# Kernel tuning notes

Measured on AMD Instinct MI355X. Metric: run time of the kernel, lower is better.

The kernel has to match this reference:

```python
import jax, jax.numpy as jnp
import numpy as np

B, S, N, F, H = 8, 12, 4096, 4, 64  # batch, seq_len, num_nodes, input_dim, hidden_dim


def setup_inputs() -> dict:
    key = jax.random.key(0)
    ks = jax.random.split(key, 16)
    sc = 0.05
    adj = jax.random.uniform(ks[0], (N, N), jnp.float32) * (2.0 / N)  # ~row-normalized Laplacian
    return {
        "X": jax.random.normal(ks[1], (B, S, N, F), jnp.float32),
        "adj": adj,
        "struc_emb": jax.random.normal(ks[2], (N, H), jnp.float32),
        "W1": jax.random.normal(ks[3], (H + F, 3 * H), jnp.float32) * sc,
        "b1": jnp.ones((3 * H,), jnp.float32),  # bias=1.0 init in graph_conv1
        "W2": jax.random.normal(ks[4], (H + F, H), jnp.float32) * sc,
        "b2": jnp.zeros((H,), jnp.float32),
        "W_ih": jax.random.normal(ks[5], (4 * H, H), jnp.float32) * sc,
        "W_hh": jax.random.normal(ks[6], (4 * H, H), jnp.float32) * sc,
        "b_ih": jnp.zeros((4 * H,), jnp.float32),
        "b_hh": jnp.zeros((4 * H,), jnp.float32),
        "D1": jax.random.normal(ks[7], (H, H // 2), jnp.float32) * sc,
        "bd1": jnp.zeros((H // 2,), jnp.float32),
        "D2": jax.random.normal(ks[8], (H // 2, 1), jnp.float32) * sc,
        "bd2": jnp.zeros((1,), jnp.float32),
    }


def _graph_conv(adj, x_t, h_flat, W, b, out_dim):
    # x_t: [B,N,F]; h_flat: [B, N*H]
    h = h_flat.reshape(B, N, H)
    cat = jnp.concatenate([x_t, h], axis=-1)            # [B,N,F+H]
    a = jnp.einsum('mn,bnf->bmf', adj, cat)             # laplacian diffusion
    out = a @ W + b                                     # [B,N,out_dim]
    return out.reshape(B, N * out_dim)


def reference(X, adj, struc_emb, W1, b1, W2, b2, W_ih, W_hh, b_ih, b_hh, D1, bd1, D2, bd2):
    # ---- encoder: TGTCCellLSTM unrolled over time (cell_state never updated, as in source) ----
    h0 = jnp.broadcast_to(struc_emb.reshape(1, N * H), (B, N * H))
    c0 = h0  # cell returns old cell_state, so it stays the struc_emb forever (faithful)

    def enc_step(h, x_t):
        g = jax.nn.sigmoid(_graph_conv(adj, x_t, h, W1, b1, 3 * H))   # [B, N*3H]
        f, i, o = jnp.split(g, 3, axis=1)                             # flat chunk, as in torch code
        conv = _graph_conv(adj, x_t, h, W2, b2, H)                    # [B, N*H]
        c = f * c0 + i * jnp.tanh(conv)
        h_new = o * jnp.tanh(c)
        return h_new, None

    h_last, _ = jax.lax.scan(enc_step, h0, jnp.swapaxes(X, 0, 1))  # scan over S
    z = h_last.reshape(B, N, H)

    # ---- decoder: 1-layer LSTM fed the same z at every step, then 2-layer MLP to scalar ----
    x_dec = z.reshape(B * N, H)
    x_gates = x_dec @ W_ih.T + b_ih + b_hh  # input contribution constant across steps

    def dec_step(carry, _):
        h, c = carry
        gates = x_gates + h @ W_hh.T
        i, f, g, o = jnp.split(gates, 4, axis=1)  # torch LSTM gate order
        c = jax.nn.sigmoid(f) * c + jax.nn.sigmoid(i) * jnp.tanh(g)
        h = jax.nn.sigmoid(o) * jnp.tanh(c)
        return (h, c), h

    zeros = jnp.zeros((B * N, H), X.dtype)
    _, hs = jax.lax.scan(dec_step, (zeros, zeros), None, length=S)  # [S, B*N, H]
    hs = jnp.swapaxes(hs, 0, 1)                                      # [B*N, S, H]
    d = jax.nn.relu(hs @ D1 + bd1) @ D2 + bd2                        # [B*N, S, 1]
    recon = d.reshape(B, S, N)  # flat reshape from (B*N, S), matching torch reshape semantics
    return (z, recon)
```

## Files before the change

### kernel.cpp

```cpp
#include <hip/hip_runtime.h>
#include <cstdint>
#include <cstddef>


typedef unsigned short u16;
typedef short s8v __attribute__((ext_vector_type(8)));
typedef unsigned short h8v __attribute__((ext_vector_type(8)));
typedef float f4v __attribute__((ext_vector_type(4)));
typedef int   i4v __attribute__((ext_vector_type(4)));

__device__ __forceinline__ u16 f2bf(float x){
  union { float f; uint32_t u; } v; v.f = x;
  uint32_t r = v.u + 0x7FFFu + ((v.u >> 16) & 1u);
  return (u16)(r >> 16);
}
__device__ __forceinline__ float bf2f(u16 x){
  union { uint32_t u; float f; } v; v.u = ((uint32_t)x) << 16; return v.f;
}
__device__ __forceinline__ float frcp(float x){ return __builtin_amdgcn_rcpf(x); }
__device__ __forceinline__ float fsig(float x){ return frcp(1.0f + __expf(-x)); }
__device__ __forceinline__ float ftanh(float x){ return 1.0f - 2.0f * frcp(1.0f + __expf(2.0f * x)); }
__device__ __forceinline__ int8_t f2i8(float x){
  int v = (int)rintf(x);
  v = v > 127 ? 127 : (v < -127 ? -127 : v);
  return (int8_t)v;
}

typedef const __attribute__((address_space(1))) unsigned int* gp_t;
typedef __attribute__((address_space(3))) unsigned int* lp_t;
__device__ __forceinline__ void glds16(const void* g, void* l){
  __builtin_amdgcn_global_load_lds((gp_t)g, (lp_t)l, 16, 0, 0);
}

__global__ __launch_bounds__(256)
void gemm_s1_i8(const int8_t* __restrict__ A, const int8_t* __restrict__ Bt,
                u16* __restrict__ Cpart, int Ncols, int ksl, float cscale)
{
  __shared__ int8_t As[2 * 128 * 128];
  __shared__ int8_t Bs[2 * 128 * 128];
  const int t  = threadIdx.x;
  const int l  = t & 63;
  const int w  = t >> 6;
  const int wm = (w >> 1) * 64;
  const int wc = (w & 1) * 64;
  const int mb = blockIdx.x * 128;
  const int nb = blockIdx.y * 128;
  const int k0 = blockIdx.z * ksl;

  i4v acc[4][4];
  #pragma unroll
  for (int i = 0; i < 4; ++i)
    #pragma unroll
    for (int j = 0; j < 4; ++j) acc[i][j] = (i4v)0;

  const int srow = t >> 3;
  const int gsw  = ((t & 7) ^ (srow & 7)) * 16;
  const int8_t* ab = A  + (size_t)(mb + srow) * 4096 + k0 + gsw;
  const int8_t* bb = Bt + (size_t)(nb + srow) * 4096 + k0 + gsw;

  const int rA = l & 15;
  const int lsw = l & 7;

  #pragma unroll
  for (int j = 0; j < 4; ++j) {
    glds16(ab + (size_t)(32 * j) * 4096, As + j * 4096 + t * 16);
    glds16(bb + (size_t)(32 * j) * 4096, Bs + j * 4096 + t * 16);
  }

  for (int kk = 0; kk < ksl; kk += 128) {
    const int cur = (kk >> 7) & 1;
    __syncthreads();
    if (kk + 128 < ksl) {
      const int nxt = cur ^ 1;
      #pragma unroll
      for (int j = 0; j < 4; ++j) {
        glds16(ab + (size_t)(32 * j) * 4096 + kk + 128, As + nxt * 16384 + j * 4096 + t * 16);
        glds16(bb + (size_t)(32 * j) * 4096 + kk + 128, Bs + nxt * 16384 + j * 4096 + t * 16);
      }
    }
    const int bofs = cur * 16384;
    #pragma unroll
    for (int sub = 0; sub < 2; ++sub) {
      const int kpos = ((sub * 4 + (l >> 4)) ^ lsw) * 16;
      i4v af[4], bf[4];
      #pragma unroll
      for (int mt = 0; mt < 4; ++mt)
        af[mt] = *(const i4v*)&As[bofs + (wm + mt * 16 + rA) * 128 + kpos];
      #pragma unroll
      for (int nt = 0; nt < 4; ++nt)
        bf[nt] = *(const i4v*)&Bs[bofs + (wc + nt * 16 + rA) * 128 + kpos];
      #pragma unroll
      for (int mt = 0; mt < 4; ++mt)
        #pragma unroll
        for (int nt = 0; nt < 4; ++nt)
          acc[mt][nt] = __builtin_amdgcn_mfma_i32_16x16x64_i8(af[mt], bf[nt], acc[mt][nt], 0, 0, 0);
    }
  }

  u16* Cs = Cpart + (size_t)blockIdx.z * 4096 * Ncols;
  const int colo = l & 15;
  const int rowo = (l >> 4) * 4;
  #pragma unroll
  for (int mt = 0; mt < 4; ++mt)
    #pragma unroll
    for (int nt = 0; nt < 4; ++nt)
      #pragma unroll
      for (int r = 0; r < 4; ++r) {
        int gr = mb + wm + mt * 16 + rowo + r;
        int gc = nb + wc + nt * 16 + colo;
        Cs[(size_t)gr * Ncols + gc] = f2bf((float)acc[mt][nt][r] * cscale);
      }
}

__global__ __launch_bounds__(256)
void reduceN(const u16* __restrict__ P, u16* __restrict__ O, size_t SL)
{
  size_t i = ((size_t)blockIdx.x * 256 + threadIdx.x) * 8;
  if (i >= SL) return;
  float s[8] = {0,0,0,0,0,0,0,0};
  #pragma unroll
  for (int z = 0; z < 4; ++z) {
    uint4 v = *(const uint4*)(P + z * SL + i);
    uint32_t wd[4] = {v.x, v.y, v.z, v.w};
    #pragma unroll
    for (int q = 0; q < 4; ++q) {
      union { uint32_t u; float f; } lo, hi;
      lo.u = wd[q] << 16; hi.u = wd[q] & 0xFFFF0000u;
      s[2*q] += lo.f; s[2*q+1] += hi.f;
    }
  }
  uint4 o; uint32_t* ow = (uint32_t*)&o;
  #pragma unroll
  for (int q = 0; q < 4; ++q)
    ow[q] = (uint32_t)f2bf(s[2*q]) | ((uint32_t)f2bf(s[2*q+1]) << 16);
  *(uint4*)(O + i) = o;
}

__global__ __launch_bounds__(256)
void gemm_s2(const u16* __restrict__ AH, const u16* __restrict__ AXb,
             const u16* __restrict__ WT, const float* __restrict__ b1v,
             const float* __restrict__ b2v, u16* __restrict__ G, int tstep)
{
  __shared__ u16 As[64*104];
  __shared__ u16 Bs[256*104];
  const int t = threadIdx.x;
  const int l = t & 63, w = t >> 6;
  const int wm = (w >> 1) * 32, wc0 = (w & 1) * 32;
  const int mb = blockIdx.x * 64;
  const size_t SL = 32768ull * 64;

  #pragma unroll
  for (int pass = 0; pass < 2; ++pass) {
    int idx = t + pass * 256;
    int row = idx >> 3, oct = idx & 7;
    size_t base = (size_t)(mb + row) * 64 + oct * 8;
    float s[8] = {0,0,0,0,0,0,0,0};
    #pragma unroll
    for (int z = 0; z < 4; ++z) {
      uint4 v = *(const uint4*)(AH + z * SL + base);
      uint32_t wd[4] = {v.x, v.y, v.z, v.w};
      #pragma unroll
      for (int q = 0; q < 4; ++q) {
        union { uint32_t u; float f; } lo, hi;
        lo.u = wd[q] << 16; hi.u = wd[q] & 0xFFFF0000u;
        s[2*q] += lo.f; s[2*q+1] += hi.f;
      }
    }
    uint4 o; uint32_t* ow = (uint32_t*)&o;
    #pragma unroll
    for (int q = 0; q < 4; ++q)
      ow[q] = (uint32_t)f2bf(s[2*q]) | ((uint32_t)f2bf(s[2*q+1]) << 16);
    *(uint4*)&As[row * 104 + oct * 8] = o;
  }
  {
    int row = t >> 2, q = t & 3;
    uint4 o = {0, 0, 0, 0};
    if (q == 0) {
      int r = mb + row, n = r >> 3, b = r & 7;
      const uint32_t* src = (const uint32_t*)(AXb + (size_t)n * 384 + tstep * 32 + b * 4);
      o.x = src[0]; o.y = src[1];
    }
    *(uint4*)&As[row * 104 + 64 + q * 8] = o;
  }
  #pragma unroll
  for (int pass = 0; pass < 12; ++pass) {
    int idx = t + pass * 256;
    int row = idx / 12, seg = idx - row * 12;
    *(uint4*)&Bs[row * 104 + seg * 8] = *(const uint4*)(WT + (size_t)row * 96 + seg * 8);
  }
  __syncthreads();

  const int rA = l & 15, kg = (l >> 4) * 8;
  s8v af[3][2];
  #pragma unroll
  for (int kc = 0; kc < 3; ++kc)
    #pragma unroll
    for (int mt = 0; mt < 2; ++mt)
      af[kc][mt] = *(const s8v*)&As[(wm + mt * 16 + rA) * 104 + kc * 32 + kg];

  const int colo = l & 15, rowo = (l >> 4) * 4;
  #pragma unroll
  for (int nb4 = 0; nb4 < 4; ++nb4) {
    const int wc = nb4 * 64 + wc0;
    f4v acc[2][2];
    #pragma unroll
    for (int i = 0; i < 2; ++i)
      #pragma unroll
      for (int j = 0; j < 2; ++j) acc[i][j] = (f4v)0.0f;
    #pragma unroll
    for (int kc = 0; kc < 3; ++kc) {
      s8v bf[2];
      #pragma unroll
      for (int nt = 0; nt < 2; ++nt)
        bf[nt] = *(const s8v*)&Bs[(wc + nt * 16 + rA) * 104 + kc * 32 + kg];
      #pragma unroll
      for (int mt = 0; mt < 2; ++mt)
        #pragma unroll
        for (int nt = 0; nt < 2; ++nt)
          acc[mt][nt] = __builtin_amdgcn_mfma_f32_16x16x32_bf16(af[kc][mt], bf[nt], acc[mt][nt], 0, 0, 0);
    }

    #pragma unroll
    for (int mt = 0; mt < 2; ++mt)
      #pragma unroll
      for (int nt = 0; nt < 2; ++nt) {
        int gc = wc + nt * 16 + colo;
        float bb = (gc < 192) ? b1v[gc] : b2v[gc - 192];
        #pragma unroll
        for (int r = 0; r < 4; ++r) {
          int gr = mb + wm + mt * 16 + rowo + r;
          int np = gr >> 3, b = gr & 7;
          float v = acc[mt][nt][r] + bb;
          size_t addr;
          u16 val;
          if (gc < 192) {
            int p = np * 192 + gc;
            int role = p >> 18;
            int k = p & 262143;
            addr = ((size_t)(role * 8 + b) << 18) + k;
            val = f2bf(fsig(v));
          } else {
            int k = np * 64 + (gc - 192);
            addr = ((size_t)(24 + b) << 18) + k;
            val = f2bf(ftanh(v));
          }
          G[addr] = val;
        }
      }
  }
}

__global__ void conv_adj_i8(const float* __restrict__ adj, int8_t* __restrict__ out){
  size_t i = ((size_t)blockIdx.x * 256 + threadIdx.x) * 4;
  float4 v = *(const float4*)(adj + i);
  const float s = 127.0f * 2048.0f;
  char4 o;
  o.x = f2i8(v.x * s); o.y = f2i8(v.y * s); o.z = f2i8(v.z * s); o.w = f2i8(v.w * s);
  *(char4*)(out + i) = o;
}

__global__ void build_w(const float* __restrict__ W1, const float* __restrict__ W2,
                        const float* __restrict__ Wih, const float* __restrict__ Whh,
                        const float* __restrict__ D1,
                        u16* __restrict__ WT, u16* __restrict__ WihB,
                        u16* __restrict__ WhhB, u16* __restrict__ D1t){
  int gid = blockIdx.x * 256 + threadIdx.x;
  if (gid < 24576) {
    int j = gid / 96, ch = gid - j * 96;
    float v = 0.0f;
    int rr = (ch < 64) ? (ch + 4) : (ch < 68 ? ch - 64 : -1);
    if (rr >= 0) v = (j < 192) ? W1[(size_t)rr * 192 + j] : W2[(size_t)rr * 64 + (j - 192)];
    WT[gid] = f2bf(v);
  } else if (gid < 40960) {
    int q = gid - 24576; WihB[q] = f2bf(Wih[q]);
  } else if (gid < 57344) {
    int q = gid - 40960; WhhB[q] = f2bf(Whh[q]);
  } else if (gid < 59392) {
    int q = gid - 57344;
    int j = q >> 6, hh = q & 63;
    D1t[q] = f2bf(D1[(size_t)hh * 32 + j]);
  }
}

__global__ void init_pb(const float* __restrict__ struc, int8_t* __restrict__ PB){
  int gid = blockIdx.x * 256 + threadIdx.x;
  int n = gid & 4095;
  int r = gid >> 12;
  int hh = r & 63;
  PB[(size_t)r * 4096 + n] = f2i8(struc[(size_t)n * 64 + hh] * 25.4f);
}

__global__ void pack_xall(const float* __restrict__ X, int8_t* __restrict__ Xp){
  int gid = blockIdx.x * 256 + threadIdx.x;
  int n = gid & 4095;
  int col = gid >> 12;
  int ts = col >> 5, r = col & 31, b = r >> 2, f = r & 3;
  Xp[(size_t)col * 4096 + n] = f2i8(X[(((size_t)(b * 12 + ts)) * 4096 + n) * 4 + f] * 25.4f);
}

__global__ __launch_bounds__(256)
void enc_update(const u16* __restrict__ G, const float* __restrict__ struc,
                int8_t* __restrict__ PB, float* __restrict__ zout,
                u16* __restrict__ zbf, int last)
{
  __shared__ uint8_t hx[64 * 40];
  const int t = threadIdx.x;
  const int b = blockIdx.x >> 7;
  const int n0 = (blockIdx.x & 127) * 32;
  const int k8 = n0 * 64 + t * 8;
  const int nloc = t >> 3;
  const int hh0 = (t & 7) * 8;

  h8v f8 = *(const h8v*)&G[((size_t)(     b) << 18) + k8];
  h8v i8_ = *(const h8v*)&G[((size_t)( 8 + b) << 18) + k8];
  h8v o8 = *(const h8v*)&G[((size_t)(16 + b) << 18) + k8];
  h8v c8 = *(const h8v*)&G[((size_t)(24 + b) << 18) + k8];
  float4 s0 = *(const float4*)&struc[k8];
  float4 s1 = *(const float4*)&struc[k8 + 4];
  float sv[8] = {s0.x, s0.y, s0.z, s0.w, s1.x, s1.y, s1.z, s1.w};

  float hv[8];
  #pragma unroll
  for (int j = 0; j < 8; ++j) {
    float c = bf2f(f8[j]) * sv[j] + bf2f(i8_[j]) * bf2f(c8[j]);
    hv[j] = bf2f(o8[j]) * ftanh(c);
    hx[(hh0 + j) * 40 + nloc] = (uint8_t)f2i8(hv[j] * 127.0f);
  }
  if (last) {
    float4 z0 = {hv[0], hv[1], hv[2], hv[3]};
    float4 z1 = {hv[4], hv[5], hv[6], hv[7]};
    *(float4*)&zout[((size_t)b << 18) + k8] = z0;
    *(float4*)&zout[((size_t)b << 18) + k8 + 4] = z1;
    h8v zb;
    #pragma unroll
    for (int j = 0; j < 8; ++j) zb[j] = f2bf(hv[j]);
    *(h8v*)&zbf[((size_t)b << 18) + k8] = zb;
  }
  __syncthreads();
  {
    int row = t >> 2, seg = t & 3;
    uint2 v = *(const uint2*)&hx[row * 40 + seg * 8];
    *(uint2*)&PB[(size_t)(b * 64 + row) * 4096 + n0 + seg * 8] = v;
  }
}

__global__ __launch_bounds__(512, 4)
void dec_fused(const u16* __restrict__ zbf, const u16* __restrict__ WihB,
               const u16* __restrict__ WhhB,
               const float* __restrict__ bih, const float* __restrict__ bhh,
               const u16* __restrict__ D1t, const float* __restrict__ bd1,
               const float* __restrict__ D2, const float* __restrict__ bd2,
               float* __restrict__ recon)
{
  __shared__ u16 whl[256 * 72];
  __shared__ u16 hl[64 * 72];
  const int t = threadIdx.x;
  const int l = t & 63;
  const int w = t >> 6;
  const int wg = w >> 1;
  const int half = w & 1;
  const int r0 = blockIdx.x * 64;
  const int rA = l & 15;
  const int kg = (l >> 4) * 8;

  for (int c = t; c < 2048; c += 512) {
    int j = c >> 3, k8 = (c & 7) * 8;
    *(uint4*)&whl[j * 72 + k8] = *(const uint4*)&WhhB[j * 64 + k8];
  }

  f4v xg[8];
  {
    s8v a0 = *(const s8v*)&zbf[(size_t)(r0 + wg * 16 + rA) * 64 + kg];
    s8v a1 = *(const s8v*)&zbf[(size_t)(r0 + wg * 16 + rA) * 64 + 32 + kg];
    #pragma unroll
    for (int j = 0; j < 8; ++j) {
      int nt = (j >> 1) * 4 + half * 2 + (j & 1);
      s8v b0 = *(const s8v*)&WihB[(nt * 16 + rA) * 64 + kg];
      s8v b1 = *(const s8v*)&WihB[(nt * 16 + rA) * 64 + 32 + kg];
      f4v a = (f4v)0.0f;
      a = __builtin_amdgcn_mfma_f32_16x16x32_bf16(a0, b0, a, 0, 0, 0);
      a = __builtin_amdgcn_mfma_f32_16x16x32_bf16(a1, b1, a, 0, 0, 0);
      float bb = bih[nt * 16 + rA] + bhh[nt * 16 + rA];
      #pragma unroll
      for (int r = 0; r < 4; ++r) xg[j][r] = a[r] + bb;
    }
  }
  s8v d1f[4];
  #pragma unroll
  for (int nt2 = 0; nt2 < 2; ++nt2)
    #pragma unroll
    for (int kc = 0; kc < 2; ++kc)
      d1f[nt2 * 2 + kc] = *(const s8v*)&D1t[(nt2 * 16 + rA) * 64 + kc * 32 + kg];
  const float bd1x = bd1[rA], bd1y = bd1[16 + rA];
  const float d2x = D2[rA], d2y = D2[16 + rA];
  const float bd2v = bd2[0];

  float cst[8];
  #pragma unroll
  for (int q = 0; q < 8; ++q) cst[q] = 0.0f;
  s8v ha0 = (s8v)0, ha1 = (s8v)0;
  __syncthreads();

  for (int s = 0; s < 12; ++s) {
    f4v acc[8];
    #pragma unroll
    for (int j = 0; j < 8; ++j) acc[j] = xg[j];
    if (s > 0) {
      #pragma unroll
      for (int j = 0; j < 8; ++j) {
        int nt = (j >> 1) * 4 + half * 2 + (j & 1);
        s8v b0 = *(const s8v*)&whl[(nt * 16 + rA) * 72 + kg];
        s8v b1 = *(const s8v*)&whl[(nt * 16 + rA) * 72 + 32 + kg];
        acc[j] = __builtin_amdgcn_mfma_f32_16x16x32_bf16(ha0, b0, acc[j], 0, 0, 0);
        acc[j] = __builtin_amdgcn_mfma_f32_16x16x32_bf16(ha1, b1, acc[j], 0, 0, 0);
      }
    }
    __syncthreads();
    #pragma unroll
    for (int ql = 0; ql < 2; ++ql) {
      int q = half * 2 + ql;
      #pragma unroll
      for (int r = 0; r < 4; ++r) {
        float i_ = fsig (acc[0 + ql][r]);
        float f_ = fsig (acc[2 + ql][r]);
        float g_ = ftanh(acc[4 + ql][r]);
        float o_ = fsig (acc[6 + ql][r]);
        float cc = f_ * cst[ql * 4 + r] + i_ * g_;
        cst[ql * 4 + r] = cc;
        float hv = o_ * ftanh(cc);
        hl[(wg * 16 + (l >> 4) * 4 + r) * 72 + q * 16 + rA] = f2bf(hv);
      }
    }
    __syncthreads();
    ha0 = *(const s8v*)&hl[(wg * 16 + rA) * 72 + kg];
    ha1 = *(const s8v*)&hl[(wg * 16 + rA) * 72 + 32 + kg];
    if (half == 0) {
      f4v m0 = (f4v)0.0f, m1 = (f4v)0.0f;
      m0 = __builtin_amdgcn_mfma_f32_16x16x32_bf16(ha0, d1f[0], m0, 0, 0, 0);
      m0 = __builtin_amdgcn_mfma_f32_16x16x32_bf16(ha1, d1f[1], m0, 0, 0, 0);
      m1 = __builtin_amdgcn_mfma_f32_16x16x32_bf16(ha0, d1f[2], m1, 0, 0, 0);
      m1 = __builtin_amdgcn_mfma_f32_16x16x32_bf16(ha1, d1f[3], m1, 0, 0, 0);
      f4v p;
      #pragma unroll
      for (int r = 0; r < 4; ++r)
        p[r] = fmaxf(m0[r] + bd1x, 0.0f) * d2x + fmaxf(m1[r] + bd1y, 0.0f) * d2y;
      #pragma unroll
      for (int mask = 1; mask < 16; mask <<= 1)
        #pragma unroll
        for (int r = 0; r < 4; ++r) p[r] += __shfl_xor(p[r], mask);
      if (rA < 4)
        recon[(size_t)(r0 + wg * 16 + (l >> 4) * 4 + rA) * 12 + s] = p[rA] + bd2v;
    }
  }
}

extern "C" void kernel_launch(void* const* d_in, const int* in_sizes, int n_in,
                              void* d_out, int out_size, void* d_ws, size_t ws_size,
                              hipStream_t stream)
{
  (void)in_sizes; (void)n_in; (void)out_size; (void)ws_size;
  const float* X     = (const float*)d_in[0];
  const float* adj   = (const float*)d_in[1];
  const float* struc = (const float*)d_in[2];
  const float* W1    = (const float*)d_in[3];
  const float* b1    = (const float*)d_in[4];
  const float* W2    = (const float*)d_in[5];
  const float* b2    = (const float*)d_in[6];
  const float* Wih   = (const float*)d_in[7];
  const float* Whh   = (const float*)d_in[8];
  const float* bih   = (const float*)d_in[9];
  const float* bhh   = (const float*)d_in[10];
  const float* D1    = (const float*)d_in[11];
  const float* bd1   = (const float*)d_in[12];
  const float* D2    = (const float*)d_in[13];
  const float* bd2   = (const float*)d_in[14];

  char* ws = (char*)d_ws;
  size_t off = 0;
  auto alloc = [&](size_t bytes){ void* p = ws + off; off += (bytes + 255) & ~(size_t)255; return p; };
  int8_t* adj_i8 = (int8_t*)alloc(4096ull * 4096);
  int8_t* PB     = (int8_t*)alloc(512ull * 4096);
  int8_t* Xp     = (int8_t*)alloc(384ull * 4096);
  u16*   AXb    = (u16*)  alloc(4096ull * 384 * 2);
  u16*   Cpart  = (u16*)  alloc(4ull * 4096 * 512 * 2);
  u16*   G      = (u16*)  alloc(4ull * 8 * 262144 * 2);
  u16*   zbf    = (u16*)  alloc(32768ull * 64 * 2);
  u16*   WT     = (u16*)  alloc(256ull * 96 * 2);
  u16*   WihB   = (u16*)  alloc(256ull * 64 * 2);
  u16*   WhhB   = (u16*)  alloc(256ull * 64 * 2);
  u16*   D1t    = (u16*)  alloc(32ull * 64 * 2);

  float* zout  = (float*)d_out;
  float* recon = (float*)d_out + 2097152;

  const float cs5 = (float)(2.0 / 4096.0 * 5.0 / (127.0 * 127.0));
  const float cs1 = (float)(2.0 / 4096.0 * 1.0 / (127.0 * 127.0));

  conv_adj_i8<<<16384, 256, 0, stream>>>(adj, adj_i8);
  build_w    <<<  232, 256, 0, stream>>>(W1, W2, Wih, Whh, D1, WT, WihB, WhhB, D1t);
  init_pb    <<< 8192, 256, 0, stream>>>(struc, PB);
  pack_xall  <<< 6144, 256, 0, stream>>>(X, Xp);
  gemm_s1_i8 <<<dim3(32, 3, 4), 256, 0, stream>>>(adj_i8, Xp, Cpart, 384, 1024, cs5);
  reduceN    <<<  768, 256, 0, stream>>>(Cpart, AXb, 4096ull * 384);

  for (int t = 0; t < 12; ++t) {
    gemm_s1_i8<<<dim3(32, 4, 4), 256, 0, stream>>>(adj_i8, PB, Cpart, 512, 1024,
                                                   t == 0 ? cs5 : cs1);
    gemm_s2<<<512, 256, 0, stream>>>(Cpart, AXb, WT, b1, b2, G, t);
    enc_update<<<1024, 256, 0, stream>>>(G, struc, PB, zout, zbf, t == 11);
  }

  dec_fused<<<512, 512, 0, stream>>>(zbf, WihB, WhhB, bih, bhh,
                                     D1t, bd1, D2, bd2, recon);
}
```

Measured before the change: 562.3 us.

## Restructure decoder LSTM kernel: per-wave gate quadrant, register-held W_hh, smaller blocks

The decoder kernel now assigns each wave one 16-column quadrant across all four gates, so each lane owns matching i/f/g/o values and keeps only four accumulators. The W_hh fragments are held in registers instead of being re-read from LDS every step. Each block handles 32 rows instead of 64, with twice as many blocks and a higher launch-bounds occupancy hint. D1 moves into a small LDS tile. Together these cut LDS traffic and usage per block to allow more concurrent waves, at the cost of redundant W_hh loads per block and extra register pressure.

```diff
diff --git a/kernel.cpp b/kernel.cpp
--- a/kernel.cpp
+++ b/kernel.cpp
@@ -344,7 +344,7 @@
   }
 }
 
-__global__ __launch_bounds__(512, 4)
+__global__ __launch_bounds__(512, 6)
 void dec_fused(const u16* __restrict__ zbf, const u16* __restrict__ WihB,
                const u16* __restrict__ WhhB,
                const float* __restrict__ bih, const float* __restrict__ bhh,
@@ -352,29 +352,37 @@
                const float* __restrict__ D2, const float* __restrict__ bd2,
                float* __restrict__ recon)
 {
-  __shared__ u16 whl[256 * 72];
-  __shared__ u16 hl[64 * 72];
+  __shared__ u16 hl[32 * 72];
+  __shared__ u16 dl[32 * 72];
   const int t = threadIdx.x;
   const int l = t & 63;
   const int w = t >> 6;
-  const int wg = w >> 1;
-  const int half = w & 1;
-  const int r0 = blockIdx.x * 64;
+  const int qt = w & 3;
+  const int wg = w >> 2;
+  const int r0 = blockIdx.x * 32;
   const int rA = l & 15;
   const int kg = (l >> 4) * 8;
 
-  for (int c = t; c < 2048; c += 512) {
-    int j = c >> 3, k8 = (c & 7) * 8;
-    *(uint4*)&whl[j * 72 + k8] = *(const uint4*)&WhhB[j * 64 + k8];
-  }
-
-  f4v xg[8];
+  if (t < 256) {
+    int row = t >> 3, chunk = t & 7;
+    *(uint4*)&dl[row * 72 + chunk * 8] = *(const uint4*)&D1t[row * 64 + chunk * 8];
+  }
+
+  s8v wb0[4], wb1[4];
+  #pragma unroll
+  for (int role = 0; role < 4; ++role) {
+    int nt = role * 4 + qt;
+    wb0[role] = *(const s8v*)&WhhB[(nt * 16 + rA) * 64 + kg];
+    wb1[role] = *(const s8v*)&WhhB[(nt * 16 + rA) * 64 + 32 + kg];
+  }
+
+  f4v xg[4];
   {
     s8v a0 = *(const s8v*)&zbf[(size_t)(r0 + wg * 16 + rA) * 64 + kg];
     s8v a1 = *(const s8v*)&zbf[(size_t)(r0 + wg * 16 + rA) * 64 + 32 + kg];
     #pragma unroll
-    for (int j = 0; j < 8; ++j) {
-      int nt = (j >> 1) * 4 + half * 2 + (j & 1);
+    for (int role = 0; role < 4; ++role) {
+      int nt = role * 4 + qt;
       s8v b0 = *(const s8v*)&WihB[(nt * 16 + rA) * 64 + kg];
       s8v b1 = *(const s8v*)&WihB[(nt * 16 + rA) * 64 + 32 + kg];
       f4v a = (f4v)0.0f;
@@ -382,64 +390,52 @@
       a = __builtin_amdgcn_mfma_f32_16x16x32_bf16(a1, b1, a, 0, 0, 0);
       float bb = bih[nt * 16 + rA] + bhh[nt * 16 + rA];
       #pragma unroll
-      for (int r = 0; r < 4; ++r) xg[j][r] = a[r] + bb;
-    }
-  }
-  s8v d1f[4];
-  #pragma unroll
-  for (int nt2 = 0; nt2 < 2; ++nt2)
-    #pragma unroll
-    for (int kc = 0; kc < 2; ++kc)
-      d1f[nt2 * 2 + kc] = *(const s8v*)&D1t[(nt2 * 16 + rA) * 64 + kc * 32 + kg];
+      for (int r = 0; r < 4; ++r) xg[role][r] = a[r] + bb;
+    }
+  }
   const float bd1x = bd1[rA], bd1y = bd1[16 + rA];
   const float d2x = D2[rA], d2y = D2[16 + rA];
   const float bd2v = bd2[0];
 
-  float cst[8];
-  #pragma unroll
-  for (int q = 0; q < 8; ++q) cst[q] = 0.0f;
+  float cst[4] = {0.0f, 0.0f, 0.0f, 0.0f};
   s8v ha0 = (s8v)0, ha1 = (s8v)0;
-  __syncthreads();
 
   for (int s = 0; s < 12; ++s) {
-    f4v acc[8];
-    #pragma unroll
-    for (int j = 0; j < 8; ++j) acc[j] = xg[j];
+    f4v acc[4];
+    #pragma unroll
+    for (int role = 0; role < 4; ++role) acc[role] = xg[role];
     if (s > 0) {
       #pragma unroll
-      for (int j = 0; j < 8; ++j) {
-        int nt = (j >> 1) * 4 + half * 2 + (j & 1);
-        s8v b0 = *(const s8v*)&whl[(nt * 16 + rA) * 72 + kg];
-        s8v b1 = *(const s8v*)&whl[(nt * 16 + rA) * 72 + 32 + kg];
-        acc[j] = __builtin_amdgcn_mfma_f32_16x16x32_bf16(ha0, b0, acc[j], 0, 0, 0);
-        acc[j] = __builtin_amdgcn_mfma_f32_16x16x32_bf16(ha1, b1, acc[j], 0, 0, 0);
+      for (int role = 0; role < 4; ++role) {
+        acc[role] = __builtin_amdgcn_mfma_f32_16x16x32_bf16(ha0, wb0[role], acc[role], 0, 0, 0);
+        acc[role] = __builtin_amdgcn_mfma_f32_16x16x32_bf16(ha1, wb1[role], acc[role], 0, 0, 0);
       }
     }
     __syncthreads();
     #pragma unroll
-    for (int ql = 0; ql < 2; ++ql) {
-      int q = half * 2 + ql;
-      #pragma unroll
-      for (int r = 0; r < 4; ++r) {
-        float i_ = fsig (acc[0 + ql][r]);
-        float f_ = fsig (acc[2 + ql][r]);
-        float g_ = ftanh(acc[4 + ql][r]);
-        float o_ = fsig (acc[6 + ql][r]);
-        float cc = f_ * cst[ql * 4 + r] + i_ * g_;
-        cst[ql * 4 + r] = cc;
-        float hv = o_ * ftanh(cc);
-        hl[(wg * 16 + (l >> 4) * 4 + r) * 72 + q * 16 + rA] = f2bf(hv);
-      }
+    for (int r = 0; r < 4; ++r) {
+      float i_ = fsig (acc[0][r]);
+      float f_ = fsig (acc[1][r]);
+      float g_ = ftanh(acc[2][r]);
+      float o_ = fsig (acc[3][r]);
+      float cc = f_ * cst[r] + i_ * g_;
+      cst[r] = cc;
+      float hv = o_ * ftanh(cc);
+      hl[(wg * 16 + (l >> 4) * 4 + r) * 72 + qt * 16 + rA] = f2bf(hv);
     }
     __syncthreads();
     ha0 = *(const s8v*)&hl[(wg * 16 + rA) * 72 + kg];
     ha1 = *(const s8v*)&hl[(wg * 16 + rA) * 72 + 32 + kg];
-    if (half == 0) {
+    if (qt == 0) {
+      s8v d1f0 = *(const s8v*)&dl[(rA) * 72 + kg];
+      s8v d1f1 = *(const s8v*)&dl[(rA) * 72 + 32 + kg];
+      s8v d1f2 = *(const s8v*)&dl[(16 + rA) * 72 + kg];
+      s8v d1f3 = *(const s8v*)&dl[(16 + rA) * 72 + 32 + kg];
       f4v m0 = (f4v)0.0f, m1 = (f4v)0.0f;
-      m0 = __builtin_amdgcn_mfma_f32_16x16x32_bf16(ha0, d1f[0], m0, 0, 0, 0);
-      m0 = __builtin_amdgcn_mfma_f32_16x16x32_bf16(ha1, d1f[1], m0, 0, 0, 0);
-      m1 = __builtin_amdgcn_mfma_f32_16x16x32_bf16(ha0, d1f[2], m1, 0, 0, 0);
-      m1 = __builtin_amdgcn_mfma_f32_16x16x32_bf16(ha1, d1f[3], m1, 0, 0, 0);
+      m0 = __builtin_amdgcn_mfma_f32_16x16x32_bf16(ha0, d1f0, m0, 0, 0, 0);
+      m0 = __builtin_amdgcn_mfma_f32_16x16x32_bf16(ha1, d1f1, m0, 0, 0, 0);
+      m1 = __builtin_amdgcn_mfma_f32_16x16x32_bf16(ha0, d1f2, m1, 0, 0, 0);
+      m1 = __builtin_amdgcn_mfma_f32_16x16x32_bf16(ha1, d1f3, m1, 0, 0, 0);
       f4v p;
       #pragma unroll
       for (int r = 0; r < 4; ++r)
@@ -510,6 +506,6 @@
     enc_update<<<1024, 256, 0, stream>>>(G, struc, PB, zout, zbf, t == 11);
   }
 
-  dec_fused<<<512, 512, 0, stream>>>(zbf, WihB, WhhB, bih, bhh,
-                                     D1t, bd1, D2, bd2, recon);
-}
+  dec_fused<<<1024, 512, 0, stream>>>(zbf, WihB, WhhB, bih, bhh,
+                                      D1t, bd1, D2, bd2, recon);
+}
```

Result: slower. 576.1 us (+2.4%).
